# Performance work log

Measured on AMD Instinct MI355X. Metric: run time of the kernel, lower is better.

Reference implementation:

```python
import jax, jax.numpy as jnp
import numpy as np

D, H, G, HD = 2048, 16, 4, 128  # d_model, num_heads, num_groups, head_dim
B, S = 2, 2048


def _rope(x):
    # x: [B, heads, S, HD]; RoPE with concat(freqs, freqs) layout (rotate_half style)
    seq = x.shape[2]
    inv_freq = 1.0 / (10000.0 ** (jnp.arange(0, HD, 2, dtype=jnp.float32) / HD))  # [HD/2]
    t = jnp.arange(seq, dtype=jnp.float32)
    freqs = t[:, None] * inv_freq[None, :]              # [S, HD/2]
    emb = jnp.concatenate([freqs, freqs], axis=-1)      # [S, HD]
    cos = jnp.cos(emb)[None, None]                      # [1,1,S,HD]
    sin = jnp.sin(emb)[None, None]
    x1, x2 = jnp.split(x, 2, axis=-1)
    rot = jnp.concatenate([-x2, x1], axis=-1)           # rotate_half
    return x * cos + rot * sin


def setup_inputs() -> dict:
    key = jax.random.key(0)
    ks = jax.random.split(key, 5)
    x = jax.random.normal(ks[0], (B, S, D), dtype=jnp.float32)
    # weights stored as [in, out] so y = x @ W (equivalent to torch Linear with W^T)
    Wq = jax.random.normal(ks[1], (D, D), dtype=jnp.float32) * 0.02
    Wk = jax.random.normal(ks[2], (D, G * HD), dtype=jnp.float32) * 0.02
    Wv = jax.random.normal(ks[3], (D, G * HD), dtype=jnp.float32) * 0.02
    Wo = jax.random.normal(ks[4], (D, D), dtype=jnp.float32) * 0.02
    # causal mask: True = masked (matches torch masked_fill semantics)
    mask = ~jnp.tril(jnp.ones((S, S), dtype=bool))[None, None]  # [1,1,S,S]
    return {"x": x, "Wq": Wq, "Wk": Wk, "Wv": Wv, "Wo": Wo, "mask": mask}


def reference(x, Wq, Wk, Wv, Wo, mask):
    b, s, _ = x.shape
    q = (x @ Wq).reshape(b, s, H, HD).transpose(0, 2, 1, 3)   # [B,H,S,HD]
    k = (x @ Wk).reshape(b, s, G, HD).transpose(0, 2, 1, 3)   # [B,G,S,HD]
    v = (x @ Wv).reshape(b, s, G, HD).transpose(0, 2, 1, 3)   # [B,G,S,HD]
    q = _rope(q)
    k = _rope(k)
    # GQA: repeat_interleave KV groups across heads
    k = jnp.repeat(k, H // G, axis=1)                         # [B,H,S,HD]
    v = jnp.repeat(v, H // G, axis=1)
    scale = jnp.float32(1.0 / np.sqrt(HD))
    scores = jnp.einsum('bhqd,bhkd->bhqk', q, k) * scale      # [B,H,S,S]
    scores = jnp.where(mask, jnp.float32(-1e9), scores)
    attn = jax.nn.softmax(scores, axis=-1)
    ctx = jnp.einsum('bhqk,bhkd->bhqd', attn, v)              # [B,H,S,HD]
    ctx = ctx.transpose(0, 2, 1, 3).reshape(b, s, D)
    return ctx @ Wo
```

## Files before the change

### kernel.cpp

```cpp
#include <hip/hip_runtime.h>
#include <hip/hip_bf16.h>
#include <math.h>

#define BB 2
#define SS 2048
#define DD 2048
#define HH 16
#define GG 4
#define HDIM 128
#define DKV (GG * HDIM)
#define MS (BB * SS)
#define QKVS 3072

typedef __attribute__((ext_vector_type(8))) short bf16x8;
typedef __attribute__((ext_vector_type(4))) float f32x4;
typedef __attribute__((ext_vector_type(4))) unsigned int u32x4;

__device__ __forceinline__ ushort f2bf(float x) {
    __hip_bfloat16 b = __float2bfloat16(x);
    return *(ushort*)&b;
}
__device__ __forceinline__ float bf2f(ushort u) {
    __hip_bfloat16 b;
    *(ushort*)&b = u;
    return __bfloat162float(b);
}

#define GLOAD_LDS(src, dst)                                                        \
    __builtin_amdgcn_global_load_lds(                                              \
        (const __attribute__((address_space(1))) unsigned int*)(src),              \
        (__attribute__((address_space(3))) unsigned int*)(dst), 16, 0, 0)

#define WAITV(n) asm volatile("s_waitcnt vmcnt(" #n ")" ::: "memory")

__global__ void cast_bf16(const float* __restrict__ X, ushort* __restrict__ O, int total8) {
    int idx = blockIdx.x * blockDim.x + threadIdx.x;
    if (idx >= total8) return;
    const float4* p = (const float4*)X + (size_t)idx * 2;
    float4 a = p[0], b = p[1];
    float v[8] = {a.x, a.y, a.z, a.w, b.x, b.y, b.z, b.w};
    ushort r[8];
#pragma unroll
    for (int j = 0; j < 8; ++j) r[j] = f2bf(v[j]);
    *((u32x4*)O + idx) = *(u32x4*)r;
}

__global__ __launch_bounds__(256) void transpose_cast(const float* __restrict__ W,
                                                      ushort* __restrict__ WT,
                                                      int K, int N) {
    __shared__ ushort tile[32][33];
    const int tx = threadIdx.x & 31, ty = threadIdx.x >> 5;
    const int n0 = blockIdx.x * 32, k0 = blockIdx.y * 32;
#pragma unroll
    for (int i = 0; i < 4; ++i)
        tile[ty + i * 8][tx] = f2bf(W[(size_t)(k0 + ty + i * 8) * N + n0 + tx]);
    __syncthreads();
#pragma unroll
    for (int i = 0; i < 4; ++i)
        WT[(size_t)(n0 + ty + i * 8) * K + k0 + tx] = tile[tx][ty + i * 8];
}

__global__ __launch_bounds__(256) void transpose_v(const ushort* __restrict__ QKV,
                                                   ushort* __restrict__ VT) {
    __shared__ ushort tile[32][33];
    const int tx = threadIdx.x & 31, ty = threadIdx.x >> 5;
    const int d0 = blockIdx.x * 32;
    const int k0 = blockIdx.y * 32;
    const int b = blockIdx.z;
#pragma unroll
    for (int i = 0; i < 4; ++i)
        tile[ty + i * 8][tx] =
            QKV[(size_t)(b * SS + k0 + ty + i * 8) * QKVS + 2560 + d0 + tx];
    __syncthreads();
    const int posl = ((tx & 12) << 1) | ((tx & 16) >> 2) | (tx & 3);
#pragma unroll
    for (int i = 0; i < 4; ++i)
        VT[((size_t)b * DKV + d0 + ty + i * 8) * SS + k0 + posl] = tile[tx][ty + i * 8];
}

template <int BN, bool OUT_BF16>
__global__ __launch_bounds__(512) void gemm8(const ushort* __restrict__ A,
                                             const ushort* __restrict__ BT,
                                             void* __restrict__ Cout,
                                             int M, int N, int K) {
    constexpr int ABUF = 128 * 32;
    constexpr int BBUF = BN * 32;
    constexpr int NWC = BN / 64;
    constexpr int NWM = 8 / NWC;
    constexpr int ROWS = 128 / NWM;
    constexpr int MFR = ROWS / 16;
    __shared__ ushort As[3 * ABUF];
    __shared__ ushort Bs[3 * BBUF];

    const int t = threadIdx.x;
    const int w = t >> 6, l = t & 63;
    const int lm = l & 15, lw = l >> 4;
    const int wr = w / NWC, wc = w % NWC;
    const int nx = gridDim.x;
    const int bid = blockIdx.y * nx + blockIdx.x;
    const int cpx = (nx * gridDim.y) >> 3;
    const int swb = (bid & 7) * cpx + (bid >> 3);
    const int bm = (swb / nx) * 128, bn = (swb % nx) * BN;

    const int NT = K >> 5;
    const int swzc = (lw ^ ((lm >> 1) & 3)) * 8;

    const int ar0 = t >> 2, ac0 = (t & 3) ^ ((ar0 >> 1) & 3);
    const ushort* a0 = A + (size_t)(bm + ar0) * K + ac0 * 8;
    const int br0 = t >> 2, bc0 = (t & 3) ^ ((br0 >> 1) & 3);
    const ushort* b0 = BT + (size_t)(bn + br0) * K + bc0 * 8;
    const int br1 = (t + 512) >> 2, bc1 = ((t + 512) & 3) ^ ((br1 >> 1) & 3);
    const ushort* b1 = BT + (size_t)(bn + br1) * K + bc1 * 8;

    auto STAGE = [&](int slot) {
        GLOAD_LDS(a0, &As[slot * ABUF + t * 8]);
        a0 += 32;
        GLOAD_LDS(b0, &Bs[slot * BBUF + t * 8]);
        b0 += 32;
        if constexpr (BN == 256) {
            GLOAD_LDS(b1, &Bs[slot * BBUF + (t + 512) * 8]);
            b1 += 32;
        }
    };

    f32x4 acc[MFR][4];
#pragma unroll
    for (int m = 0; m < MFR; ++m)
#pragma unroll
        for (int n = 0; n < 4; ++n) acc[m][n] = (f32x4){0.f, 0.f, 0.f, 0.f};

    STAGE(0);
    STAGE(1);
    int cs = 0, ps = 2;

#pragma unroll 1
    for (int kt = 0; kt < NT; ++kt) {
        if (kt + 1 < NT) {
            if constexpr (BN == 256) WAITV(3); else WAITV(2);
        } else {
            WAITV(0);
        }
        __builtin_amdgcn_s_barrier();
        if (kt + 2 < NT) STAGE(ps);

        const ushort* Ab = &As[cs * ABUF];
        const ushort* Bb = &Bs[cs * BBUF];
        bf16x8 bfr[4], af[MFR];
#pragma unroll
        for (int n = 0; n < 4; ++n)
            bfr[n] = *(const bf16x8*)&Bb[(wc * 64 + n * 16 + lm) * 32 + swzc];
#pragma unroll
        for (int i = 0; i < MFR; ++i)
            af[i] = *(const bf16x8*)&Ab[(wr * ROWS + i * 16 + lm) * 32 + swzc];
        __builtin_amdgcn_s_setprio(1);
#pragma unroll
        for (int i = 0; i < MFR; ++i)
#pragma unroll
            for (int n = 0; n < 4; ++n)
                acc[i][n] = __builtin_amdgcn_mfma_f32_16x16x32_bf16(af[i], bfr[n], acc[i][n], 0, 0, 0);
        __builtin_amdgcn_s_setprio(0);

        cs = (cs == 2) ? 0 : cs + 1;
        ps = (ps == 2) ? 0 : ps + 1;
    }

#pragma unroll
    for (int m = 0; m < MFR; ++m)
#pragma unroll
        for (int n = 0; n < 4; ++n)
#pragma unroll
            for (int r = 0; r < 4; ++r) {
                int row = bm + wr * ROWS + m * 16 + lw * 4 + r;
                int col = bn + wc * 64 + n * 16 + lm;
                if (OUT_BF16)
                    ((ushort*)Cout)[(size_t)row * N + col] = f2bf(acc[m][n][r]);
                else
                    ((float*)Cout)[(size_t)row * N + col] = acc[m][n][r];
            }
}

__global__ void rope_bf16(ushort* __restrict__ X, int total) {
    int idx = blockIdx.x * blockDim.x + threadIdx.x;
    if (idx >= total) return;
    int i = idx & 63;
    int hh = (idx >> 6) % 20;
    int row = idx / (64 * 20);
    int s = row & (SS - 1);
    int colOff = (hh < 16) ? hh * HDIM : 2048 + (hh - 16) * HDIM;
    float inv = exp2f((float)i * -0.2076205059304601f);
    float ang = (float)s * inv;
    float c, sn;
    __sincosf(ang, &sn, &c);
    size_t base = (size_t)row * QKVS + colOff + i;
    float x1 = bf2f(X[base]), x2 = bf2f(X[base + 64]);
    X[base] = f2bf(x1 * c - x2 * sn);
    X[base + 64] = f2bf(x2 * c + x1 * sn);
}

#define SCL 0.08838834764831845f
#define CEXP 0.1275296340545927f
#define THRRAW 90.50966799187809f

__global__ __launch_bounds__(512) void attn_mfma(const ushort* __restrict__ QKV,
                                                 const ushort* __restrict__ VT,
                                                 ushort* __restrict__ Ctx) {
    __shared__ ushort Ks[2][64 * 128];
    __shared__ ushort Vs[2][128 * 64];
    const int t = threadIdx.x;
    const int w = t >> 6;
    const int l = t & 63;
    const int lm = l & 15, lw = l >> 4;
    const int bid = blockIdx.x;
    const int g = bid & 3;
    const int b = (bid >> 2) & 1;
    const int within = bid >> 3;
    const int xq = within & 7;
    const int h = g * 4 + (within >> 3);
    const int swz = (lm & 7) << 3;

    const ushort* kbase = QKV + (size_t)(b * SS) * QKVS + 2048 + g * HDIM;
    const ushort* vbase = VT + ((size_t)b * DKV + g * HDIM) * SS;

    const short one_bf = (short)0x3F80;
    const bf16x8 ones = {one_bf, one_bf, one_bf, one_bf, one_bf, one_bf, one_bf, one_bf};

    const int kr0 = t >> 4, ko0 = t & 15;
    const int kr1 = (t + 512) >> 4, ko1 = (t + 512) & 15;
    const int vr0 = t >> 3, vo0 = t & 7;
    const int vr1 = (t + 512) >> 3, vo1 = (t + 512) & 7;
    ushort* kd0a = &Ks[0][t * 8];
    ushort* kd0b = &Ks[1][t * 8];
    ushort* kd1a = &Ks[0][(t + 512) * 8];
    ushort* kd1b = &Ks[1][(t + 512) * 8];
    ushort* vd0a = &Vs[0][t * 8];
    ushort* vd0b = &Vs[1][t * 8];
    ushort* vd1a = &Vs[0][(t + 512) * 8];
    ushort* vd1b = &Vs[1][(t + 512) * 8];

#pragma unroll 1
    for (int phase = 0; phase < 2; ++phase) {
        const int qt = (phase == 0) ? xq : (15 - xq);
        const int q0 = qt * 128;
        const int qw = q0 + w * 16;
        const int q = qw + lm;
        const int ntiles = 2 * qt + 2;
        const int lt = (qw + 15) >> 6;

        const ushort* ks0 = kbase + (size_t)kr0 * QKVS + ((ko0 ^ (kr0 & 7)) * 8);
        const ushort* ks1 = kbase + (size_t)kr1 * QKVS + ((ko1 ^ (kr1 & 7)) * 8);
        const ushort* vs0 = vbase + (size_t)vr0 * SS + ((vo0 ^ (vr0 & 7)) * 8);
        const ushort* vs1 = vbase + (size_t)vr1 * SS + ((vo1 ^ (vr1 & 7)) * 8);

        bf16x8 qa[4];
        {
            const ushort* qp = QKV + (size_t)(b * SS + qw + lm) * QKVS + h * HDIM + lw * 8;
#pragma unroll
            for (int kk = 0; kk < 4; ++kk)
                qa[kk] = *(const bf16x8*)(qp + kk * 32);
        }

        f32x4 acc[8];
#pragma unroll
        for (int d = 0; d < 8; ++d) acc[d] = (f32x4){0.f, 0.f, 0.f, 0.f};
        f32x4 accl = (f32x4){0.f, 0.f, 0.f, 0.f};
        float m = -INFINITY;

        GLOAD_LDS(ks0, kd0a);
        GLOAD_LDS(ks1, kd1a);
        ks0 += 64 * QKVS;
        ks1 += 64 * QKVS;
        GLOAD_LDS(vs0, vd0a);
        GLOAD_LDS(vs1, vd1a);
        vs0 += 64;
        vs1 += 64;
        asm volatile("s_waitcnt vmcnt(0)" ::: "memory");
        __builtin_amdgcn_s_barrier();

#pragma unroll 1
        for (int tile = 0; tile < ntiles; ++tile) {
            const int cur = tile & 1;
            const int kv0 = tile * 64;
            const bool more = (tile + 1 < ntiles);
            if (more) {
                GLOAD_LDS(ks0, cur ? kd0a : kd0b);
                GLOAD_LDS(ks1, cur ? kd1a : kd1b);
                ks0 += 64 * QKVS;
                ks1 += 64 * QKVS;
                GLOAD_LDS(vs0, cur ? vd0a : vd0b);
                GLOAD_LDS(vs1, cur ? vd1a : vd1b);
                vs0 += 64;
                vs1 += 64;
            }

            if (tile <= lt) {
                f32x4 sfT[4];
#pragma unroll
                for (int kvb = 0; kvb < 4; ++kvb) sfT[kvb] = (f32x4){0.f, 0.f, 0.f, 0.f};
                __builtin_amdgcn_s_setprio(1);
#pragma unroll
                for (int kvb = 0; kvb < 4; ++kvb)
#pragma unroll
                    for (int kk = 0; kk < 4; ++kk) {
                        bf16x8 kb = *(const bf16x8*)&Ks[cur][(kvb * 16 + lm) * 128 + ((kk * 32 + lw * 8) ^ swz)];
                        sfT[kvb] = __builtin_amdgcn_mfma_f32_16x16x32_bf16(kb, qa[kk], sfT[kvb], 0, 0, 0);
                    }
                __builtin_amdgcn_s_setprio(0);

                if (tile == lt) {
#pragma unroll
                    for (int kvb = 0; kvb < 4; ++kvb)
#pragma unroll
                        for (int r = 0; r < 4; ++r) {
                            int kv = kv0 + kvb * 16 + lw * 4 + r;
                            if (kv > q) sfT[kvb][r] = -INFINITY;
                        }
                }

                float rm = fmaxf(fmaxf(sfT[0][0], sfT[0][1]), fmaxf(sfT[0][2], sfT[0][3]));
#pragma unroll
                for (int kvb = 1; kvb < 4; ++kvb) {
                    rm = fmaxf(rm, fmaxf(fmaxf(sfT[kvb][0], sfT[kvb][1]),
                                         fmaxf(sfT[kvb][2], sfT[kvb][3])));
                }
                rm = fmaxf(rm, __shfl_xor(rm, 16));
                rm = fmaxf(rm, __shfl_xor(rm, 32));

                bool stable = (rm - m <= THRRAW);
                if (!__all((int)stable)) {
                    float mn = fmaxf(m, rm);
                    float alpha_l = exp2f((m - mn) * CEXP);
                    m = mn;
                    float ar[4];
#pragma unroll
                    for (int r = 0; r < 4; ++r)
                        ar[r] = __shfl(alpha_l, (l & 48) | (lw * 4 + r));
#pragma unroll
                    for (int d = 0; d < 8; ++d) {
                        acc[d][0] *= ar[0];
                        acc[d][1] *= ar[1];
                        acc[d][2] *= ar[2];
                        acc[d][3] *= ar[3];
                    }
                    accl[0] *= ar[0];
                    accl[1] *= ar[1];
                    accl[2] *= ar[2];
                    accl[3] *= ar[3];
                }

                bf16x8 pa[2];
                float mC = m * CEXP;
#pragma unroll
                for (int kvb = 0; kvb < 4; ++kvb)
#pragma unroll
                    for (int r = 0; r < 4; ++r) {
                        float pv = exp2f(fmaf(sfT[kvb][r], CEXP, -mC));
                        pa[kvb >> 1][(kvb & 1) * 4 + r] = (short)f2bf(pv);
                    }

                __builtin_amdgcn_s_setprio(1);
#pragma unroll
                for (int kks = 0; kks < 2; ++kks) {
                    accl = __builtin_amdgcn_mfma_f32_16x16x32_bf16(pa[kks], ones, accl, 0, 0, 0);
#pragma unroll
                    for (int dcol = 0; dcol < 8; ++dcol) {
                        bf16x8 vb = *(const bf16x8*)&Vs[cur][(dcol * 16 + lm) * 64 + ((kks * 32 + lw * 8) ^ swz)];
                        acc[dcol] = __builtin_amdgcn_mfma_f32_16x16x32_bf16(pa[kks], vb, acc[dcol], 0, 0, 0);
                    }
                }
                __builtin_amdgcn_s_setprio(0);
            }

            if (more) {
                asm volatile("s_waitcnt vmcnt(0)" ::: "memory");
                __builtin_amdgcn_s_barrier();
            }
        }

        float rinv[4];
#pragma unroll
        for (int r = 0; r < 4; ++r) rinv[r] = 1.f / accl[r];
        ushort* cp = Ctx + (size_t)(b * SS + qw) * DD + h * HDIM;
#pragma unroll
        for (int d = 0; d < 8; ++d)
#pragma unroll
            for (int r = 0; r < 4; ++r)
                cp[(size_t)(lw * 4 + r) * DD + d * 16 + lm] = f2bf(acc[d][r] * rinv[r]);
        __builtin_amdgcn_s_barrier();
    }
}

extern "C" void kernel_launch(void* const* d_in, const int* in_sizes, int n_in,
                              void* d_out, int out_size, void* d_ws, size_t ws_size,
                              hipStream_t stream) {
    const float* x  = (const float*)d_in[0];
    const float* Wq = (const float*)d_in[1];
    const float* Wk = (const float*)d_in[2];
    const float* Wv = (const float*)d_in[3];
    const float* Wo = (const float*)d_in[4];
    float* out = (float*)d_out;

    ushort* xh    = (ushort*)d_ws;
    ushort* QKV   = xh + (size_t)MS * DD;
    ushort* VTb   = QKV + (size_t)MS * QKVS;
    ushort* WqkvT = VTb + (size_t)MS * DKV;
    ushort* WoT   = WqkvT + (size_t)QKVS * DD;
    ushort* Ch    = xh;

    dim3 blk(256);
    int nx8 = MS * DD / 8;
    cast_bf16<<<(nx8 + 255) / 256, 256, 0, stream>>>(x, xh, nx8);

    transpose_cast<<<dim3(DD / 32, DD / 32), blk, 0, stream>>>(Wq, WqkvT, DD, DD);
    transpose_cast<<<dim3(DKV / 32, DD / 32), blk, 0, stream>>>(Wk, WqkvT + (size_t)DD * DD, DD, DKV);
    transpose_cast<<<dim3(DKV / 32, DD / 32), blk, 0, stream>>>(Wv, WqkvT + (size_t)(DD + DKV) * DD, DD, DKV);

    gemm8<256, true><<<dim3(QKVS / 256, MS / 128), dim3(512), 0, stream>>>(xh, WqkvT, QKV, MS, QKVS, DD);

    int nrope = MS * 20 * 64;
    rope_bf16<<<(nrope + 255) / 256, 256, 0, stream>>>(QKV, nrope);

    transpose_v<<<dim3(DKV / 32, SS / 32, BB), blk, 0, stream>>>(QKV, VTb);

    attn_mfma<<<dim3(256), dim3(512), 0, stream>>>(QKV, VTb, Ch);

    transpose_cast<<<dim3(DD / 32, DD / 32), blk, 0, stream>>>(Wo, WoT, DD, DD);
    gemm8<128, false><<<dim3(DD / 128, MS / 128), dim3(512), 0, stream>>>(Ch, WoT, out, MS, DD, DD);
}
```

Before: 210.4 us.

## Shrink attention query tile to 64 rows with 256-thread blocks and more blocks

The attention kernel now uses 64-row query tiles, 256 threads (4 waves) per block and a 512-block grid instead of 128-row tiles with 512 threads and 256 blocks. Each thread issues four async K/V loads per tile instead of two, and the per-wave causal skip check is gone because each 64-row tile lines up with the 64-wide KV tiles. The aim is better load balance and occupancy across CUs and less wasted causal work. In exchange, K/V tiles are fetched from global memory twice as often relative to the query work done per block, so reuse drops.

```diff
diff --git a/kernel.cpp b/kernel.cpp
--- a/kernel.cpp
+++ b/kernel.cpp
@@ -201,7 +201,7 @@
 #define CEXP 0.1275296340545927f
 #define THRRAW 90.50966799187809f
 
-__global__ __launch_bounds__(512) void attn_mfma(const ushort* __restrict__ QKV,
+__global__ __launch_bounds__(256) void attn_mfma(const ushort* __restrict__ QKV,
                                                  const ushort* __restrict__ VT,
                                                  ushort* __restrict__ Ctx) {
     __shared__ ushort Ks[2][64 * 128];
@@ -214,8 +214,8 @@
     const int g = bid & 3;
     const int b = (bid >> 2) & 1;
     const int within = bid >> 3;
-    const int xq = within & 7;
-    const int h = g * 4 + (within >> 3);
+    const int xq = within & 15;
+    const int h = g * 4 + (within >> 4);
     const int swz = (lm & 7) << 3;
 
     const ushort* kbase = QKV + (size_t)(b * SS) * QKVS + 2048 + g * HDIM;
@@ -224,32 +224,27 @@
     const short one_bf = (short)0x3F80;
     const bf16x8 ones = {one_bf, one_bf, one_bf, one_bf, one_bf, one_bf, one_bf, one_bf};
 
-    const int kr0 = t >> 4, ko0 = t & 15;
-    const int kr1 = (t + 512) >> 4, ko1 = (t + 512) & 15;
-    const int vr0 = t >> 3, vo0 = t & 7;
-    const int vr1 = (t + 512) >> 3, vo1 = (t + 512) & 7;
-    ushort* kd0a = &Ks[0][t * 8];
-    ushort* kd0b = &Ks[1][t * 8];
-    ushort* kd1a = &Ks[0][(t + 512) * 8];
-    ushort* kd1b = &Ks[1][(t + 512) * 8];
-    ushort* vd0a = &Vs[0][t * 8];
-    ushort* vd0b = &Vs[1][t * 8];
-    ushort* vd1a = &Vs[0][(t + 512) * 8];
-    ushort* vd1b = &Vs[1][(t + 512) * 8];
+    ushort* ksb = &Ks[0][0];
+    ushort* vsb = &Vs[0][0];
 
 #pragma unroll 1
     for (int phase = 0; phase < 2; ++phase) {
-        const int qt = (phase == 0) ? xq : (15 - xq);
-        const int q0 = qt * 128;
+        const int qt = (phase == 0) ? xq : (31 - xq);
+        const int q0 = qt * 64;
         const int qw = q0 + w * 16;
         const int q = qw + lm;
-        const int ntiles = 2 * qt + 2;
-        const int lt = (qw + 15) >> 6;
-
-        const ushort* ks0 = kbase + (size_t)kr0 * QKVS + ((ko0 ^ (kr0 & 7)) * 8);
-        const ushort* ks1 = kbase + (size_t)kr1 * QKVS + ((ko1 ^ (kr1 & 7)) * 8);
-        const ushort* vs0 = vbase + (size_t)vr0 * SS + ((vo0 ^ (vr0 & 7)) * 8);
-        const ushort* vs1 = vbase + (size_t)vr1 * SS + ((vo1 ^ (vr1 & 7)) * 8);
+        const int ntiles = qt + 1;
+
+        const ushort* ks[4];
+        const ushort* vs[4];
+#pragma unroll
+        for (int it = 0; it < 4; ++it) {
+            int c = t + it * 256;
+            int kr = c >> 4, ko = c & 15;
+            ks[it] = kbase + (size_t)kr * QKVS + ((ko ^ (kr & 7)) * 8);
+            int vr = c >> 3, vo = c & 7;
+            vs[it] = vbase + (size_t)vr * SS + ((vo ^ (vr & 7)) * 8);
+        }
 
         bf16x8 qa[4];
         {
@@ -265,14 +260,13 @@
         f32x4 accl = (f32x4){0.f, 0.f, 0.f, 0.f};
         float m = -INFINITY;
 
-        GLOAD_LDS(ks0, kd0a);
-        GLOAD_LDS(ks1, kd1a);
-        ks0 += 64 * QKVS;
-        ks1 += 64 * QKVS;
-        GLOAD_LDS(vs0, vd0a);
-        GLOAD_LDS(vs1, vd1a);
-        vs0 += 64;
-        vs1 += 64;
+#pragma unroll
+        for (int it = 0; it < 4; ++it) {
+            GLOAD_LDS(ks[it], ksb + (t + it * 256) * 8);
+            ks[it] += 64 * QKVS;
+            GLOAD_LDS(vs[it], vsb + (t + it * 256) * 8);
+            vs[it] += 64;
+        }
         asm volatile("s_waitcnt vmcnt(0)" ::: "memory");
         __builtin_amdgcn_s_barrier();
 
@@ -282,93 +276,91 @@
             const int kv0 = tile * 64;
             const bool more = (tile + 1 < ntiles);
             if (more) {
-                GLOAD_LDS(ks0, cur ? kd0a : kd0b);
-                GLOAD_LDS(ks1, cur ? kd1a : kd1b);
-                ks0 += 64 * QKVS;
-                ks1 += 64 * QKVS;
-                GLOAD_LDS(vs0, cur ? vd0a : vd0b);
-                GLOAD_LDS(vs1, cur ? vd1a : vd1b);
-                vs0 += 64;
-                vs1 += 64;
-            }
-
-            if (tile <= lt) {
-                f32x4 sfT[4];
-#pragma unroll
-                for (int kvb = 0; kvb < 4; ++kvb) sfT[kvb] = (f32x4){0.f, 0.f, 0.f, 0.f};
-                __builtin_amdgcn_s_setprio(1);
+                ushort* kd = ksb + (cur ^ 1) * (64 * 128);
+                ushort* vd = vsb + (cur ^ 1) * (128 * 64);
+#pragma unroll
+                for (int it = 0; it < 4; ++it) {
+                    GLOAD_LDS(ks[it], kd + (t + it * 256) * 8);
+                    ks[it] += 64 * QKVS;
+                    GLOAD_LDS(vs[it], vd + (t + it * 256) * 8);
+                    vs[it] += 64;
+                }
+            }
+
+            f32x4 sfT[4];
+#pragma unroll
+            for (int kvb = 0; kvb < 4; ++kvb) sfT[kvb] = (f32x4){0.f, 0.f, 0.f, 0.f};
+            __builtin_amdgcn_s_setprio(1);
+#pragma unroll
+            for (int kvb = 0; kvb < 4; ++kvb)
+#pragma unroll
+                for (int kk = 0; kk < 4; ++kk) {
+                    bf16x8 kb = *(const bf16x8*)&Ks[cur][(kvb * 16 + lm) * 128 + ((kk * 32 + lw * 8) ^ swz)];
+                    sfT[kvb] = __builtin_amdgcn_mfma_f32_16x16x32_bf16(kb, qa[kk], sfT[kvb], 0, 0, 0);
+                }
+            __builtin_amdgcn_s_setprio(0);
+
+            if (tile == ntiles - 1) {
 #pragma unroll
                 for (int kvb = 0; kvb < 4; ++kvb)
 #pragma unroll
-                    for (int kk = 0; kk < 4; ++kk) {
-                        bf16x8 kb = *(const bf16x8*)&Ks[cur][(kvb * 16 + lm) * 128 + ((kk * 32 + lw * 8) ^ swz)];
-                        sfT[kvb] = __builtin_amdgcn_mfma_f32_16x16x32_bf16(kb, qa[kk], sfT[kvb], 0, 0, 0);
+                    for (int r = 0; r < 4; ++r) {
+                        int kv = kv0 + kvb * 16 + lw * 4 + r;
+                        if (kv > q) sfT[kvb][r] = -INFINITY;
                     }
-                __builtin_amdgcn_s_setprio(0);
-
-                if (tile == lt) {
-#pragma unroll
-                    for (int kvb = 0; kvb < 4; ++kvb)
-#pragma unroll
-                        for (int r = 0; r < 4; ++r) {
-                            int kv = kv0 + kvb * 16 + lw * 4 + r;
-                            if (kv > q) sfT[kvb][r] = -INFINITY;
-                        }
+            }
+
+            float rm = fmaxf(fmaxf(sfT[0][0], sfT[0][1]), fmaxf(sfT[0][2], sfT[0][3]));
+#pragma unroll
+            for (int kvb = 1; kvb < 4; ++kvb)
+                rm = fmaxf(rm, fmaxf(fmaxf(sfT[kvb][0], sfT[kvb][1]),
+                                     fmaxf(sfT[kvb][2], sfT[kvb][3])));
+            rm = fmaxf(rm, __shfl_xor(rm, 16));
+            rm = fmaxf(rm, __shfl_xor(rm, 32));
+
+            bool stable = (rm - m <= THRRAW);
+            if (!__all((int)stable)) {
+                float mn = fmaxf(m, rm);
+                float alpha_l = exp2f((m - mn) * CEXP);
+                m = mn;
+                float ar[4];
+#pragma unroll
+                for (int r = 0; r < 4; ++r)
+                    ar[r] = __shfl(alpha_l, (l & 48) | (lw * 4 + r));
+#pragma unroll
+                for (int d = 0; d < 8; ++d) {
+                    acc[d][0] *= ar[0];
+                    acc[d][1] *= ar[1];
+                    acc[d][2] *= ar[2];
+                    acc[d][3] *= ar[3];
                 }
-
-                float rm = fmaxf(fmaxf(sfT[0][0], sfT[0][1]), fmaxf(sfT[0][2], sfT[0][3]));
-#pragma unroll
-                for (int kvb = 1; kvb < 4; ++kvb) {
-                    rm = fmaxf(rm, fmaxf(fmaxf(sfT[kvb][0], sfT[kvb][1]),
-                                         fmaxf(sfT[kvb][2], sfT[kvb][3])));
+                accl[0] *= ar[0];
+                accl[1] *= ar[1];
+                accl[2] *= ar[2];
+                accl[3] *= ar[3];
+            }
+
+            bf16x8 pa[2];
+            float mC = m * CEXP;
+#pragma unroll
+            for (int kvb = 0; kvb < 4; ++kvb)
+#pragma unroll
+                for (int r = 0; r < 4; ++r) {
+                    float pv = exp2f(fmaf(sfT[kvb][r], CEXP, -mC));
+                    pa[kvb >> 1][(kvb & 1) * 4 + r] = (short)f2bf(pv);
                 }
-                rm = fmaxf(rm, __shfl_xor(rm, 16));
-                rm = fmaxf(rm, __shfl_xor(rm, 32));
-
-                bool stable = (rm - m <= THRRAW);
-                if (!__all((int)stable)) {
-                    float mn = fmaxf(m, rm);
-                    float alpha_l = exp2f((m - mn) * CEXP);
-                    m = mn;
-                    float ar[4];
-#pragma unroll
-                    for (int r = 0; r < 4; ++r)
-                        ar[r] = __shfl(alpha_l, (l & 48) | (lw * 4 + r));
-#pragma unroll
-                    for (int d = 0; d < 8; ++d) {
-                        acc[d][0] *= ar[0];
-                        acc[d][1] *= ar[1];
-                        acc[d][2] *= ar[2];
-                        acc[d][3] *= ar[3];
-                    }
-                    accl[0] *= ar[0];
-                    accl[1] *= ar[1];
-                    accl[2] *= ar[2];
-                    accl[3] *= ar[3];
+
+            __builtin_amdgcn_s_setprio(1);
+#pragma unroll
+            for (int kks = 0; kks < 2; ++kks) {
+                accl = __builtin_amdgcn_mfma_f32_16x16x32_bf16(pa[kks], ones, accl, 0, 0, 0);
+#pragma unroll
+                for (int dcol = 0; dcol < 8; ++dcol) {
+                    bf16x8 vb = *(const bf16x8*)&Vs[cur][(dcol * 16 + lm) * 64 + ((kks * 32 + lw * 8) ^ swz)];
+                    acc[dcol] = __builtin_amdgcn_mfma_f32_16x16x32_bf16(pa[kks], vb, acc[dcol], 0, 0, 0);
                 }
-
-                bf16x8 pa[2];
-                float mC = m * CEXP;
-#pragma unroll
-                for (int kvb = 0; kvb < 4; ++kvb)
-#pragma unroll
-                    for (int r = 0; r < 4; ++r) {
-                        float pv = exp2f(fmaf(sfT[kvb][r], CEXP, -mC));
-                        pa[kvb >> 1][(kvb & 1) * 4 + r] = (short)f2bf(pv);
-                    }
-
-                __builtin_amdgcn_s_setprio(1);
-#pragma unroll
-                for (int kks = 0; kks < 2; ++kks) {
-                    accl = __builtin_amdgcn_mfma_f32_16x16x32_bf16(pa[kks], ones, accl, 0, 0, 0);
-#pragma unroll
-                    for (int dcol = 0; dcol < 8; ++dcol) {
-                        bf16x8 vb = *(const bf16x8*)&Vs[cur][(dcol * 16 + lm) * 64 + ((kks * 32 + lw * 8) ^ swz)];
-                        acc[dcol] = __builtin_amdgcn_mfma_f32_16x16x32_bf16(pa[kks], vb, acc[dcol], 0, 0, 0);
-                    }
-                }
-                __builtin_amdgcn_s_setprio(0);
-            }
+            }
+            __builtin_amdgcn_s_setprio(0);
 
             if (more) {
                 asm volatile("s_waitcnt vmcnt(0)" ::: "memory");
@@ -421,7 +413,7 @@
 
     transpose_v<<<dim3(DKV / 32, SS / 32, BB), blk, 0, stream>>>(QKV, VTb);
 
-    attn_mfma<<<dim3(256), dim3(512), 0, stream>>>(QKV, VTb, Ch);
+    attn_mfma<<<dim3(512), dim3(256), 0, stream>>>(QKV, VTb, Ch);
 
     transpose_cast<<<dim3(DD / 32, DD / 32), blk, 0, stream>>>(Wo, WoT, DD, DD);
     gemm8<128, false><<<dim3(DD / 128, MS / 128), dim3(512), 0, stream>>>(Ch, WoT, out, MS, DD, DD);
```

Result: no change. 210.1 us (-0.2%).

## Triple-buffer attention K/V tiles and merge QKV weight transposes into one launch

Applied to the files above, without the earlier changes.

The attention kernel moves from double to triple buffering of K/V tiles in LDS. Two tiles are prefetched ahead, and a partial vmcnt wait plus a single barrier at the top of each iteration replace the full drain at the end of each iteration. This lets global loads overlap more with the MFMA work, at the cost of 96KB of LDS per block. Separately, the three Wq/Wk/Wv transpose-cast launches are merged into one 3D-grid launch, with early exit for the out-of-range blocks of the narrower K/V weights, to cut launch overhead.

```diff
diff --git a/kernel.cpp b/kernel.cpp
--- a/kernel.cpp
+++ b/kernel.cpp
@@ -43,6 +43,28 @@
 #pragma unroll
     for (int j = 0; j < 8; ++j) r[j] = f2bf(v[j]);
     *((u32x4*)O + idx) = *(u32x4*)r;
+}
+
+__global__ __launch_bounds__(256) void transpose_cast3(const float* __restrict__ Wq,
+                                                       const float* __restrict__ Wk,
+                                                       const float* __restrict__ Wv,
+                                                       ushort* __restrict__ WqkvT) {
+    __shared__ ushort tile[32][33];
+    const int z = blockIdx.z;
+    if (z > 0 && blockIdx.x >= DKV / 32) return;
+    const float* W = (z == 0) ? Wq : (z == 1) ? Wk : Wv;
+    ushort* WT = WqkvT + ((z == 0) ? (size_t)0 : (z == 1) ? (size_t)DD * DD
+                                                          : (size_t)(DD + DKV) * DD);
+    const int N = (z == 0) ? DD : DKV;
+    const int tx = threadIdx.x & 31, ty = threadIdx.x >> 5;
+    const int n0 = blockIdx.x * 32, k0 = blockIdx.y * 32;
+#pragma unroll
+    for (int i = 0; i < 4; ++i)
+        tile[ty + i * 8][tx] = f2bf(W[(size_t)(k0 + ty + i * 8) * N + n0 + tx]);
+    __syncthreads();
+#pragma unroll
+    for (int i = 0; i < 4; ++i)
+        WT[(size_t)(n0 + ty + i * 8) * DD + k0 + tx] = tile[tx][ty + i * 8];
 }
 
 __global__ __launch_bounds__(256) void transpose_cast(const float* __restrict__ W,
@@ -204,8 +226,8 @@
 __global__ __launch_bounds__(512) void attn_mfma(const ushort* __restrict__ QKV,
                                                  const ushort* __restrict__ VT,
                                                  ushort* __restrict__ Ctx) {
-    __shared__ ushort Ks[2][64 * 128];
-    __shared__ ushort Vs[2][128 * 64];
+    __shared__ ushort Ks[3][64 * 128];
+    __shared__ ushort Vs[3][128 * 64];
     const int t = threadIdx.x;
     const int w = t >> 6;
     const int l = t & 63;
@@ -228,14 +250,6 @@
     const int kr1 = (t + 512) >> 4, ko1 = (t + 512) & 15;
     const int vr0 = t >> 3, vo0 = t & 7;
     const int vr1 = (t + 512) >> 3, vo1 = (t + 512) & 7;
-    ushort* kd0a = &Ks[0][t * 8];
-    ushort* kd0b = &Ks[1][t * 8];
-    ushort* kd1a = &Ks[0][(t + 512) * 8];
-    ushort* kd1b = &Ks[1][(t + 512) * 8];
-    ushort* vd0a = &Vs[0][t * 8];
-    ushort* vd0b = &Vs[1][t * 8];
-    ushort* vd1a = &Vs[0][(t + 512) * 8];
-    ushort* vd1b = &Vs[1][(t + 512) * 8];
 
 #pragma unroll 1
     for (int phase = 0; phase < 2; ++phase) {
@@ -251,6 +265,17 @@
         const ushort* vs0 = vbase + (size_t)vr0 * SS + ((vo0 ^ (vr0 & 7)) * 8);
         const ushort* vs1 = vbase + (size_t)vr1 * SS + ((vo1 ^ (vr1 & 7)) * 8);
 
+        auto STAGE = [&](int slot) {
+            GLOAD_LDS(ks0, &Ks[slot][t * 8]);
+            ks0 += 64 * QKVS;
+            GLOAD_LDS(ks1, &Ks[slot][(t + 512) * 8]);
+            ks1 += 64 * QKVS;
+            GLOAD_LDS(vs0, &Vs[slot][t * 8]);
+            vs0 += 64;
+            GLOAD_LDS(vs1, &Vs[slot][(t + 512) * 8]);
+            vs1 += 64;
+        };
+
         bf16x8 qa[4];
         {
             const ushort* qp = QKV + (size_t)(b * SS + qw + lm) * QKVS + h * HDIM + lw * 8;
@@ -265,32 +290,20 @@
         f32x4 accl = (f32x4){0.f, 0.f, 0.f, 0.f};
         float m = -INFINITY;
 
-        GLOAD_LDS(ks0, kd0a);
-        GLOAD_LDS(ks1, kd1a);
-        ks0 += 64 * QKVS;
-        ks1 += 64 * QKVS;
-        GLOAD_LDS(vs0, vd0a);
-        GLOAD_LDS(vs1, vd1a);
-        vs0 += 64;
-        vs1 += 64;
-        asm volatile("s_waitcnt vmcnt(0)" ::: "memory");
-        __builtin_amdgcn_s_barrier();
+        STAGE(0);
+        STAGE(1);
+        int cs = 0, ps = 2;
 
 #pragma unroll 1
         for (int tile = 0; tile < ntiles; ++tile) {
-            const int cur = tile & 1;
             const int kv0 = tile * 64;
-            const bool more = (tile + 1 < ntiles);
-            if (more) {
-                GLOAD_LDS(ks0, cur ? kd0a : kd0b);
-                GLOAD_LDS(ks1, cur ? kd1a : kd1b);
-                ks0 += 64 * QKVS;
-                ks1 += 64 * QKVS;
-                GLOAD_LDS(vs0, cur ? vd0a : vd0b);
-                GLOAD_LDS(vs1, cur ? vd1a : vd1b);
-                vs0 += 64;
-                vs1 += 64;
+            if (tile + 1 < ntiles) {
+                WAITV(4);
+            } else {
+                WAITV(0);
             }
+            __builtin_amdgcn_s_barrier();
+            if (tile + 2 < ntiles) STAGE(ps);
 
             if (tile <= lt) {
                 f32x4 sfT[4];
@@ -301,7 +314,7 @@
                 for (int kvb = 0; kvb < 4; ++kvb)
 #pragma unroll
                     for (int kk = 0; kk < 4; ++kk) {
-                        bf16x8 kb = *(const bf16x8*)&Ks[cur][(kvb * 16 + lm) * 128 + ((kk * 32 + lw * 8) ^ swz)];
+                        bf16x8 kb = *(const bf16x8*)&Ks[cs][(kvb * 16 + lm) * 128 + ((kk * 32 + lw * 8) ^ swz)];
                         sfT[kvb] = __builtin_amdgcn_mfma_f32_16x16x32_bf16(kb, qa[kk], sfT[kvb], 0, 0, 0);
                     }
                 __builtin_amdgcn_s_setprio(0);
@@ -318,10 +331,9 @@
 
                 float rm = fmaxf(fmaxf(sfT[0][0], sfT[0][1]), fmaxf(sfT[0][2], sfT[0][3]));
 #pragma unroll
-                for (int kvb = 1; kvb < 4; ++kvb) {
+                for (int kvb = 1; kvb < 4; ++kvb)
                     rm = fmaxf(rm, fmaxf(fmaxf(sfT[kvb][0], sfT[kvb][1]),
                                          fmaxf(sfT[kvb][2], sfT[kvb][3])));
-                }
                 rm = fmaxf(rm, __shfl_xor(rm, 16));
                 rm = fmaxf(rm, __shfl_xor(rm, 32));
 
@@ -363,17 +375,15 @@
                     accl = __builtin_amdgcn_mfma_f32_16x16x32_bf16(pa[kks], ones, accl, 0, 0, 0);
 #pragma unroll
                     for (int dcol = 0; dcol < 8; ++dcol) {
-                        bf16x8 vb = *(const bf16x8*)&Vs[cur][(dcol * 16 + lm) * 64 + ((kks * 32 + lw * 8) ^ swz)];
+                        bf16x8 vb = *(const bf16x8*)&Vs[cs][(dcol * 16 + lm) * 64 + ((kks * 32 + lw * 8) ^ swz)];
                         acc[dcol] = __builtin_amdgcn_mfma_f32_16x16x32_bf16(pa[kks], vb, acc[dcol], 0, 0, 0);
                     }
                 }
                 __builtin_amdgcn_s_setprio(0);
             }
 
-            if (more) {
-                asm volatile("s_waitcnt vmcnt(0)" ::: "memory");
-                __builtin_amdgcn_s_barrier();
-            }
+            cs = (cs == 2) ? 0 : cs + 1;
+            ps = (ps == 2) ? 0 : ps + 1;
         }
 
         float rinv[4];
@@ -410,9 +420,7 @@
     int nx8 = MS * DD / 8;
     cast_bf16<<<(nx8 + 255) / 256, 256, 0, stream>>>(x, xh, nx8);
 
-    transpose_cast<<<dim3(DD / 32, DD / 32), blk, 0, stream>>>(Wq, WqkvT, DD, DD);
-    transpose_cast<<<dim3(DKV / 32, DD / 32), blk, 0, stream>>>(Wk, WqkvT + (size_t)DD * DD, DD, DKV);
-    transpose_cast<<<dim3(DKV / 32, DD / 32), blk, 0, stream>>>(Wv, WqkvT + (size_t)(DD + DKV) * DD, DD, DKV);
+    transpose_cast3<<<dim3(DD / 32, DD / 32, 3), blk, 0, stream>>>(Wq, Wk, Wv, WqkvT);
 
     gemm8<256, true><<<dim3(QKVS / 256, MS / 128), dim3(512), 0, stream>>>(xh, WqkvT, QKV, MS, QKVS, DD);
 
```

After: 213.3 us. About the same (+1.4%).
